# Optimization experiments

Hardware: AMD Instinct MI355X
Metric: run time of the kernel (lower is better)

The kernel has to match this reference:

```python
import jax
import jax.numpy as jnp
import numpy as np

DIM = 1024        # obs dim == latent dim (invertible affine map)
TIME = 4096       # number of timesteps


def setup_inputs() -> dict:
    key = jax.random.key(0)
    ks = jax.random.split(key, 7)
    H = DIM
    scale_hh = 1.0 / np.sqrt(H)
    inp = {
        "ts": jnp.arange(TIME, dtype=jnp.float32),
        "u0": jax.random.normal(ks[0], (H,), dtype=jnp.float32),
        "W_ih": jax.random.normal(ks[1], (3 * H, 1), dtype=jnp.float32) * scale_hh,
        "W_hh": jax.random.normal(ks[2], (3 * H, H), dtype=jnp.float32) * scale_hh,
        "b_ih": jax.random.normal(ks[3], (3 * H,), dtype=jnp.float32) * 0.01,
        "b_hh": jax.random.normal(ks[4], (3 * H,), dtype=jnp.float32) * 0.01,
        # well-conditioned invertible affine map: A = I + 0.02 * N(0,1)
        "A": jnp.eye(H, dtype=jnp.float32)
        + 0.02 * jax.random.normal(ks[5], (H, H), dtype=jnp.float32),
        "c": jax.random.normal(ks[6], (H,), dtype=jnp.float32) * 0.1,
    }
    return inp


def reference(ts, u0, W_ih, W_hh, b_ih, b_hh, A, c):
    # make_initial_state: to_latent(u0) = inverse affine map
    h0 = jnp.linalg.solve(A, u0 - c)  # [H]

    # dim_control is None -> control = zeros(1); input gates are step-invariant
    control = jnp.zeros((1,), dtype=u0.dtype)
    ig = W_ih @ control + b_ih  # [3H]
    ir, iz, inn = jnp.split(ig, 3)

    def gru_cell(h):
        hg = W_hh @ h + b_hh  # [3H]
        hr, hz, hn = jnp.split(hg, 3)
        r = jax.nn.sigmoid(ir + hr)
        z = jax.nn.sigmoid(iz + hz)
        n = jnp.tanh(inn + r * hn)
        return (1.0 - z) * n + z * h

    def body_fn(h_prev, t):
        h_next = gru_cell(h_prev)
        return h_next, h_next

    _, hs_ = jax.lax.scan(body_fn, h0, ts[1:])  # [T-1, H]
    hs = jnp.concatenate((h0[None, :], hs_), axis=0)  # [T, H]

    # vmapped to_obs: affine map obs = A @ h + c
    return hs @ A.T + c  # [T, H]
```

## Files before the change

### kernel.cpp

```cpp
#include <hip/hip_runtime.h>

#define H 1024
#define T 4096
#define GR 64
#define NBLK 256
#define TPB 1024
#define WPB 16
#define SOLVE_ITERS 48
#define FINAL_E (SOLVE_ITERS + T - 1)

typedef float v2f __attribute__((ext_vector_type(2)));
typedef unsigned long long u64;
typedef u64 u64x2 __attribute__((ext_vector_type(2)));

__device__ __forceinline__ float sigmoidf_(float x) { return 1.0f / (1.0f + __expf(-x)); }
__device__ __forceinline__ float tanh_fast_(float x) { return 2.0f * sigmoidf_(2.0f * x) - 1.0f; }

__device__ __forceinline__ u64 pack_(float v, unsigned salt) {
    const unsigned lo = __float_as_uint(v);
    return ((u64)(lo ^ salt) << 32) | lo;
}
__device__ __forceinline__ int valid_(u64 v, unsigned salt) {
    return (((unsigned)(v >> 32)) ^ (unsigned)v) == salt;
}
__device__ __forceinline__ void pub_(u64* p, u64 pk) {
    __hip_atomic_store(p, pk, __ATOMIC_RELAXED, __HIP_MEMORY_SCOPE_AGENT);
}
__device__ __forceinline__ u64x2 load16_coh_(const u64* p) {
    u64x2 v;
    asm volatile("global_load_dwordx4 %0, %1, off sc0 sc1\n\ts_waitcnt vmcnt(0)"
                 : "=v"(v) : "v"(p) : "memory");
    return v;
}
__device__ __forceinline__ u64 load8_coh_(const u64* p) {
    u64 v;
    asm volatile("global_load_dwordx2 %0, %1, off sc0 sc1\n\ts_waitcnt vmcnt(0)"
                 : "=v"(v) : "v"(p) : "memory");
    return v;
}
__device__ __forceinline__ v2f poll2_(const u64* pb, int e, int j2) {
    const unsigned salt = ~(unsigned)e;
    const u64* p = pb + (size_t)(e & 1) * H + j2;
    for (;;) {
        const u64x2 v = load16_coh_(p);
        if (valid_(v.x, salt) && valid_(v.y, salt)) {
            v2f r;
            r.x = __uint_as_float((unsigned)v.x);
            r.y = __uint_as_float((unsigned)v.y);
            return r;
        }
    }
}

__device__ __forceinline__ void rnn_block_(
    const float* __restrict__ u0, const float* __restrict__ W_hh,
    const float* __restrict__ b_ih, const float* __restrict__ b_hh,
    const float* __restrict__ Amat, const float* __restrict__ c,
    float* __restrict__ out, u64* __restrict__ pbuf)
{
    __shared__ float hlds[2][H];
    __shared__ u64 hpub[2][WPB];
    const int tid  = threadIdx.x;
    const int lane = tid & 63;
    const int wave = tid >> 6;
    const int b    = blockIdx.x;
    const int j    = b * WPB + wave;

    float wr[16], wz[16], wn[16];
    {
        const float* pr = W_hh + (size_t)j * H;
        const float* pz = W_hh + (size_t)(H + j) * H;
        const float* pn = W_hh + (size_t)(2 * H + j) * H;
#pragma unroll
        for (int k = 0; k < 16; ++k) {
            wr[k] = pr[lane + 64 * k];
            wz[k] = pz[lane + 64 * k];
            wn[k] = pn[lane + 64 * k];
        }
    }
    const float br  = b_ih[j]         + b_hh[j];
    const float bz  = b_ih[H + j]     + b_hh[H + j];
    const float bin = b_ih[2 * H + j];
    const float bhn = b_hh[2 * H + j];
    const float bj  = u0[j] - c[j];

    if (lane == 0) hpub[0][wave] = pack_(bj, ~0u);
    __syncthreads();
    if (tid < WPB) pub_(&pbuf[(size_t)b * WPB + tid], hpub[0][tid]);

    const float* arow = Amat + (size_t)j * H;
    for (int r = 1; r <= SOLVE_ITERS; ++r) {
        const int pp = (r - 1) & 1;
        if (tid < 512) {
            if ((tid >> 3) == b) {
                const int w0 = 2 * (tid & 7);
                hlds[pp][2 * tid]     = __uint_as_float((unsigned)hpub[pp][w0]);
                hlds[pp][2 * tid + 1] = __uint_as_float((unsigned)hpub[pp][w0 + 1]);
            } else {
                *(v2f*)&hlds[pp][2 * tid] = poll2_(pbuf, r - 1, 2 * tid);
            }
        }
        __syncthreads();
        float acc = 0.f;
#pragma unroll
        for (int k = 0; k < 16; ++k) acc += arow[lane + 64 * k] * hlds[pp][lane + 64 * k];
#pragma unroll
        for (int m = 32; m >= 1; m >>= 1) acc += __shfl_xor(acc, m, 64);
        if (lane == 0) {
            const float hn = bj + hlds[pp][j] - acc;
            hpub[r & 1][wave] = pack_(hn, ~(unsigned)r);
            if (r == SOLVE_ITERS) out[j] = hn;
        }
        __syncthreads();
        if (tid < WPB)
            pub_(&pbuf[(size_t)(r & 1) * H + b * WPB + tid], hpub[r & 1][tid]);
    }

    for (int t = 1; t < T; ++t) {
        const int e  = SOLVE_ITERS + t;
        const int pp = (e - 1) & 1;
        if (tid < 512) {
            if ((tid >> 3) == b) {
                const int w0 = 2 * (tid & 7);
                hlds[pp][2 * tid]     = __uint_as_float((unsigned)hpub[pp][w0]);
                hlds[pp][2 * tid + 1] = __uint_as_float((unsigned)hpub[pp][w0 + 1]);
            } else {
                *(v2f*)&hlds[pp][2 * tid] = poll2_(pbuf, e - 1, 2 * tid);
            }
        }
        __syncthreads();

        float hv[16];
#pragma unroll
        for (int k = 0; k < 16; ++k) hv[k] = hlds[pp][lane + 64 * k];
        float ar = 0.f, az = 0.f, an = 0.f;
#pragma unroll
        for (int k = 0; k < 16; ++k) {
            ar += wr[k] * hv[k];
            az += wz[k] * hv[k];
            an += wn[k] * hv[k];
        }
#pragma unroll
        for (int m = 32; m >= 1; m >>= 1) {
            ar += __shfl_xor(ar, m, 64);
            az += __shfl_xor(az, m, 64);
            an += __shfl_xor(an, m, 64);
        }
        if (lane == 0) {
            const float r2  = sigmoidf_(br + ar);
            const float z2  = sigmoidf_(bz + az);
            const float n2  = tanh_fast_(bin + r2 * (an + bhn));
            const float hn2 = (1.f - z2) * n2 + z2 * hlds[pp][j];
            hpub[e & 1][wave] = pack_(hn2, ~(unsigned)e);
            out[(size_t)t * H + j] = hn2;
        }
        __syncthreads();
        if (tid < WPB)
            pub_(&pbuf[(size_t)(e & 1) * H + b * WPB + tid], hpub[e & 1][tid]);
    }
}

__device__ __forceinline__ void burner_(const u64* __restrict__ pbuf,
                                        float* __restrict__ dummy)
{
    const unsigned salt = ~(unsigned)FINAL_E;
    const u64* flag = &pbuf[(size_t)(FINAL_E & 1) * H];
    const float a = 1.0000001f, b = 1e-7f;
    float x0 = (float)threadIdx.x * 1e-3f + 0.1f;
    float x1 = x0 + 0.25f, x2 = x0 + 0.5f, x3 = x0 + 0.75f;
#pragma unroll 1
    for (int it = 0; it < (1 << 15); ++it) {
#pragma unroll
        for (int k = 0; k < 64; ++k) {
            x0 = __builtin_fmaf(x0, a, b);
            x1 = __builtin_fmaf(x1, a, b);
            x2 = __builtin_fmaf(x2, a, b);
            x3 = __builtin_fmaf(x3, a, b);
        }
        if ((it & 7) == 7) {
            const u64 v = load8_coh_(flag);
            if (valid_(v, salt)) break;
        }
    }
    if (__float_as_uint(x0 + x1 + x2 + x3) == 0xDEADBEEFu)
        dummy[threadIdx.x] = x0;
}

__global__ __launch_bounds__(TPB) void rnn_burn_kernel(
    const float* __restrict__ u0, const float* __restrict__ W_hh,
    const float* __restrict__ b_ih, const float* __restrict__ b_hh,
    const float* __restrict__ A, const float* __restrict__ c,
    float* __restrict__ out, u64* __restrict__ pbuf, float* __restrict__ dummy)
{
    if (blockIdx.x < GR)
        rnn_block_(u0, W_hh, b_ih, b_hh, A, c, out, pbuf);
    else
        burner_(pbuf, dummy);
}

#define ORT 8
__global__ __launch_bounds__(256) void obs_kernel(
    const float* __restrict__ A, const float* __restrict__ c,
    float* __restrict__ out)
{
    __shared__ float hl[ORT][H];
    __shared__ float at[64][65];
    const int tid = threadIdx.x;
    const int t0  = blockIdx.x * ORT;
    for (int i = tid; i < ORT * H / 4; i += 256)
        ((float4*)&hl[0][0])[i] = ((const float4*)(out + (size_t)t0 * H))[i];
    __syncthreads();
    const int li = tid & 63, lt2 = (tid >> 6) * 2;
    for (int it = 0; it < 16; ++it) {
        const int i0 = it * 64;
        float acc0 = c[i0 + li], acc1 = acc0;
        for (int jt = 0; jt < 16; ++jt) {
            const int j0 = jt * 64;
            __syncthreads();
            {
                const int r0 = tid >> 4, cq = (tid & 15) * 4;
                for (int rr = r0; rr < 64; rr += 16) {
                    const float4 v = *(const float4*)&A[(size_t)(i0 + rr) * H + j0 + cq];
                    at[rr][cq] = v.x; at[rr][cq + 1] = v.y;
                    at[rr][cq + 2] = v.z; at[rr][cq + 3] = v.w;
                }
            }
            __syncthreads();
#pragma unroll 16
            for (int jx = 0; jx < 64; ++jx) {
                const float av = at[li][jx];
                acc0 += av * hl[lt2][j0 + jx];
                acc1 += av * hl[lt2 + 1][j0 + jx];
            }
        }
        out[(size_t)(t0 + lt2) * H + i0 + li]     = acc0;
        out[(size_t)(t0 + lt2 + 1) * H + i0 + li] = acc1;
    }
}

extern "C" void kernel_launch(void* const* d_in, const int* in_sizes, int n_in,
                              void* d_out, int out_size, void* d_ws, size_t ws_size,
                              hipStream_t stream) {
    const float* u0   = (const float*)d_in[1];
    const float* W_hh = (const float*)d_in[3];
    const float* b_ih = (const float*)d_in[4];
    const float* b_hh = (const float*)d_in[5];
    const float* A    = (const float*)d_in[6];
    const float* c    = (const float*)d_in[7];
    float* out   = (float*)d_out;
    u64*   pbuf  = (u64*)d_ws;
    float* dummy = (float*)((char*)d_ws + 16384);

    hipLaunchKernelGGL(rnn_burn_kernel, dim3(NBLK), dim3(TPB), 0, stream,
                       u0, W_hh, b_ih, b_hh, A, c, out, pbuf, dummy);
    hipLaunchKernelGGL(obs_kernel, dim3(T / ORT), dim3(256), 0, stream,
                       A, c, out);
}
```

Baseline: 9.915 ms.

## Replace block barriers with salted LDS mailboxes and per-chunk polling

Removes both __syncthreads per timestep. Polling threads write salted 64-bit values into LDS mailboxes, and each wave consumes 64-element chunks as soon as they become valid, accumulating FMAs out of order. Publishing to global memory is done by wave 0 spinning on per-wave salted slots in LDS instead of waiting at a barrier. This aims to cut barrier latency from the serial critical path, but adds LDS spin traffic, bounded timeout loops and a dependence on volatile LDS ordering.

```diff
diff --git a/kernel.cpp b/kernel.cpp
--- a/kernel.cpp
+++ b/kernel.cpp
@@ -38,19 +38,6 @@
                  : "=v"(v) : "v"(p) : "memory");
     return v;
 }
-__device__ __forceinline__ v2f poll2_(const u64* pb, int e, int j2) {
-    const unsigned salt = ~(unsigned)e;
-    const u64* p = pb + (size_t)(e & 1) * H + j2;
-    for (;;) {
-        const u64x2 v = load16_coh_(p);
-        if (valid_(v.x, salt) && valid_(v.y, salt)) {
-            v2f r;
-            r.x = __uint_as_float((unsigned)v.x);
-            r.y = __uint_as_float((unsigned)v.y);
-            return r;
-        }
-    }
-}
 
 __device__ __forceinline__ void rnn_block_(
     const float* __restrict__ u0, const float* __restrict__ W_hh,
@@ -58,13 +45,90 @@
     const float* __restrict__ Amat, const float* __restrict__ c,
     float* __restrict__ out, u64* __restrict__ pbuf)
 {
-    __shared__ float hlds[2][H];
+    __shared__ u64 hmb[2][H];
     __shared__ u64 hpub[2][WPB];
     const int tid  = threadIdx.x;
     const int lane = tid & 63;
     const int wave = tid >> 6;
-    const int b    = blockIdx.x;
-    const int j    = b * WPB + wave;
+    const int bb   = blockIdx.x;
+    const int j    = bb * WPB + wave;
+    const int jl   = j & 63;
+    const int jm   = j >> 6;
+
+    for (int i = tid; i < 2 * H; i += TPB) ((u64*)hmb)[i] = 0ull;
+    if (tid < 2 * WPB) ((u64*)hpub)[tid] = 0ull;
+    __syncthreads();
+
+    const float br  = b_ih[j]         + b_hh[j];
+    const float bz  = b_ih[H + j]     + b_hh[H + j];
+    const float bin = b_ih[2 * H + j];
+    const float bhn = b_hh[2 * H + j];
+    const float bj  = u0[j] - c[j];
+
+    if (lane == 0) hpub[0][wave] = pack_(bj, ~0u);
+    if (wave == 0 && lane < WPB) {
+        const volatile u64* hp = hpub[0];
+        u64 v = hp[lane];
+        int g = 0;
+        while (!valid_(v, ~0u) && ++g < (1 << 22)) v = hp[lane];
+        pub_(&pbuf[(size_t)bb * WPB + lane], v);
+    }
+
+    {
+        float wa[16];
+        const float* arow = Amat + (size_t)j * H;
+#pragma unroll
+        for (int m = 0; m < 16; ++m) wa[m] = arow[lane + 64 * m];
+
+        for (int r = 1; r <= SOLVE_ITERS; ++r) {
+            const int ev = r - 1;
+            const int pc = ev & 1;
+            const unsigned psalt = ~(unsigned)ev;
+            if (tid < 512) {
+                const u64* gp = pbuf + (size_t)pc * H + 2 * tid;
+                u64x2 v; int g = 0;
+                for (;;) {
+                    v = load16_coh_(gp);
+                    if ((valid_(v.x, psalt) && valid_(v.y, psalt)) || ++g > (1 << 20)) break;
+                }
+                hmb[pc][2 * tid]     = v.x;
+                hmb[pc][2 * tid + 1] = v.y;
+            }
+            float acc = 0.f, hself = 0.f;
+            unsigned ok = 0; int g = 0;
+            const volatile u64* hl = hmb[pc];
+            u64 tv[16];
+            while (ok != 0xFFFFu && ++g < (1 << 20)) {
+#pragma unroll
+                for (int m = 0; m < 16; ++m)
+                    if (!(ok >> m & 1)) tv[m] = hl[lane + (m << 6)];
+#pragma unroll
+                for (int m = 0; m < 16; ++m)
+                    if (!(ok >> m & 1) && valid_(tv[m], psalt)) {
+                        ok |= 1u << m;
+                        const float h = __uint_as_float((unsigned)tv[m]);
+                        acc = __builtin_fmaf(wa[m], h, acc);
+                        if (m == jm) hself = h;
+                    }
+            }
+#pragma unroll
+            for (int m = 32; m >= 1; m >>= 1) acc += __shfl_xor(acc, m, 64);
+            const float hpj = __shfl(hself, jl, 64);
+            const float hn  = bj + hpj - acc;
+            if (lane == 0) {
+                hpub[r & 1][wave] = pack_(hn, ~(unsigned)r);
+                if (r == SOLVE_ITERS) out[j] = hn;
+            }
+            if (wave == 0 && lane < WPB) {
+                const volatile u64* hp = hpub[r & 1];
+                const unsigned esalt = ~(unsigned)r;
+                u64 v = hp[lane];
+                int gg = 0;
+                while (!valid_(v, esalt) && ++gg < (1 << 22)) v = hp[lane];
+                pub_(&pbuf[(size_t)(r & 1) * H + bb * WPB + lane], v);
+            }
+        }
+    }
 
     float wr[16], wz[16], wn[16];
     {
@@ -72,73 +136,46 @@
         const float* pz = W_hh + (size_t)(H + j) * H;
         const float* pn = W_hh + (size_t)(2 * H + j) * H;
 #pragma unroll
-        for (int k = 0; k < 16; ++k) {
-            wr[k] = pr[lane + 64 * k];
-            wz[k] = pz[lane + 64 * k];
-            wn[k] = pn[lane + 64 * k];
-        }
-    }
-    const float br  = b_ih[j]         + b_hh[j];
-    const float bz  = b_ih[H + j]     + b_hh[H + j];
-    const float bin = b_ih[2 * H + j];
-    const float bhn = b_hh[2 * H + j];
-    const float bj  = u0[j] - c[j];
-
-    if (lane == 0) hpub[0][wave] = pack_(bj, ~0u);
-    __syncthreads();
-    if (tid < WPB) pub_(&pbuf[(size_t)b * WPB + tid], hpub[0][tid]);
-
-    const float* arow = Amat + (size_t)j * H;
-    for (int r = 1; r <= SOLVE_ITERS; ++r) {
-        const int pp = (r - 1) & 1;
-        if (tid < 512) {
-            if ((tid >> 3) == b) {
-                const int w0 = 2 * (tid & 7);
-                hlds[pp][2 * tid]     = __uint_as_float((unsigned)hpub[pp][w0]);
-                hlds[pp][2 * tid + 1] = __uint_as_float((unsigned)hpub[pp][w0 + 1]);
-            } else {
-                *(v2f*)&hlds[pp][2 * tid] = poll2_(pbuf, r - 1, 2 * tid);
-            }
-        }
-        __syncthreads();
-        float acc = 0.f;
-#pragma unroll
-        for (int k = 0; k < 16; ++k) acc += arow[lane + 64 * k] * hlds[pp][lane + 64 * k];
-#pragma unroll
-        for (int m = 32; m >= 1; m >>= 1) acc += __shfl_xor(acc, m, 64);
-        if (lane == 0) {
-            const float hn = bj + hlds[pp][j] - acc;
-            hpub[r & 1][wave] = pack_(hn, ~(unsigned)r);
-            if (r == SOLVE_ITERS) out[j] = hn;
-        }
-        __syncthreads();
-        if (tid < WPB)
-            pub_(&pbuf[(size_t)(r & 1) * H + b * WPB + tid], hpub[r & 1][tid]);
+        for (int m = 0; m < 16; ++m) {
+            wr[m] = pr[lane + 64 * m];
+            wz[m] = pz[lane + 64 * m];
+            wn[m] = pn[lane + 64 * m];
+        }
     }
 
     for (int t = 1; t < T; ++t) {
         const int e  = SOLVE_ITERS + t;
-        const int pp = (e - 1) & 1;
+        const int ev = e - 1;
+        const int pc = ev & 1;
+        const unsigned psalt = ~(unsigned)ev;
         if (tid < 512) {
-            if ((tid >> 3) == b) {
-                const int w0 = 2 * (tid & 7);
-                hlds[pp][2 * tid]     = __uint_as_float((unsigned)hpub[pp][w0]);
-                hlds[pp][2 * tid + 1] = __uint_as_float((unsigned)hpub[pp][w0 + 1]);
-            } else {
-                *(v2f*)&hlds[pp][2 * tid] = poll2_(pbuf, e - 1, 2 * tid);
-            }
-        }
-        __syncthreads();
-
-        float hv[16];
-#pragma unroll
-        for (int k = 0; k < 16; ++k) hv[k] = hlds[pp][lane + 64 * k];
-        float ar = 0.f, az = 0.f, an = 0.f;
-#pragma unroll
-        for (int k = 0; k < 16; ++k) {
-            ar += wr[k] * hv[k];
-            az += wz[k] * hv[k];
-            an += wn[k] * hv[k];
+            const u64* gp = pbuf + (size_t)pc * H + 2 * tid;
+            u64x2 v; int g = 0;
+            for (;;) {
+                v = load16_coh_(gp);
+                if ((valid_(v.x, psalt) && valid_(v.y, psalt)) || ++g > (1 << 20)) break;
+            }
+            hmb[pc][2 * tid]     = v.x;
+            hmb[pc][2 * tid + 1] = v.y;
+        }
+        float ar = 0.f, az = 0.f, an = 0.f, hself = 0.f;
+        unsigned ok = 0; int g = 0;
+        const volatile u64* hl = hmb[pc];
+        u64 tv[16];
+        while (ok != 0xFFFFu && ++g < (1 << 20)) {
+#pragma unroll
+            for (int m = 0; m < 16; ++m)
+                if (!(ok >> m & 1)) tv[m] = hl[lane + (m << 6)];
+#pragma unroll
+            for (int m = 0; m < 16; ++m)
+                if (!(ok >> m & 1) && valid_(tv[m], psalt)) {
+                    ok |= 1u << m;
+                    const float h = __uint_as_float((unsigned)tv[m]);
+                    ar = __builtin_fmaf(wr[m], h, ar);
+                    az = __builtin_fmaf(wz[m], h, az);
+                    an = __builtin_fmaf(wn[m], h, an);
+                    if (m == jm) hself = h;
+                }
         }
 #pragma unroll
         for (int m = 32; m >= 1; m >>= 1) {
@@ -146,17 +183,23 @@
             az += __shfl_xor(az, m, 64);
             an += __shfl_xor(an, m, 64);
         }
+        const float hpj = __shfl(hself, jl, 64);
+        const float r2  = sigmoidf_(br + ar);
+        const float z2  = sigmoidf_(bz + az);
+        const float n2  = tanh_fast_(bin + r2 * (an + bhn));
+        const float hn2 = (1.f - z2) * n2 + z2 * hpj;
         if (lane == 0) {
-            const float r2  = sigmoidf_(br + ar);
-            const float z2  = sigmoidf_(bz + az);
-            const float n2  = tanh_fast_(bin + r2 * (an + bhn));
-            const float hn2 = (1.f - z2) * n2 + z2 * hlds[pp][j];
             hpub[e & 1][wave] = pack_(hn2, ~(unsigned)e);
             out[(size_t)t * H + j] = hn2;
         }
-        __syncthreads();
-        if (tid < WPB)
-            pub_(&pbuf[(size_t)(e & 1) * H + b * WPB + tid], hpub[e & 1][tid]);
+        if (wave == 0 && lane < WPB) {
+            const volatile u64* hp = hpub[e & 1];
+            const unsigned esalt = ~(unsigned)e;
+            u64 v = hp[lane];
+            int gg = 0;
+            while (!valid_(v, esalt) && ++gg < (1 << 22)) v = hp[lane];
+            pub_(&pbuf[(size_t)(e & 1) * H + bb * WPB + lane], v);
+        }
     }
 }
 
```

New measurement: 25.69 ms. +159.1%, slower.

## Pin recurrent blocks to one XCC and poll with L2-scope loads

Applied to the files above, without the earlier changes.

Doubles the grid and reads the hardware XCC id so that only blocks landing on XCC 0 claim the 64 recurrent slots through an atomic counter; all other blocks run the burner. With every per-step producer and consumer sharing one L2, most polls use L2-coherent loads (sc0) and only every eighth poll is a system-coherent load. The aim is to cut cross-XCC coherence latency on each of the thousands of serial steps. Risks: it assumes exactly 64 co-resident blocks reach XCC 0, the counter is never reset between calls, and the poll loop is now bounded, so it can fall through and return stale values.

```diff
diff --git a/kernel.cpp b/kernel.cpp
--- a/kernel.cpp
+++ b/kernel.cpp
@@ -2,8 +2,7 @@
 
 #define H 1024
 #define T 4096
-#define GR 64
-#define NBLK 256
+#define NBLK 512
 #define TPB 1024
 #define WPB 16
 #define SOLVE_ITERS 48
@@ -32,39 +31,45 @@
                  : "=v"(v) : "v"(p) : "memory");
     return v;
 }
+__device__ __forceinline__ u64x2 load16_l2_(const u64* p) {
+    u64x2 v;
+    asm volatile("global_load_dwordx4 %0, %1, off sc0\n\ts_waitcnt vmcnt(0)"
+                 : "=v"(v) : "v"(p) : "memory");
+    return v;
+}
 __device__ __forceinline__ u64 load8_coh_(const u64* p) {
     u64 v;
     asm volatile("global_load_dwordx2 %0, %1, off sc0 sc1\n\ts_waitcnt vmcnt(0)"
                  : "=v"(v) : "v"(p) : "memory");
     return v;
 }
+
 __device__ __forceinline__ v2f poll2_(const u64* pb, int e, int j2) {
     const unsigned salt = ~(unsigned)e;
     const u64* p = pb + (size_t)(e & 1) * H + j2;
-    for (;;) {
-        const u64x2 v = load16_coh_(p);
-        if (valid_(v.x, salt) && valid_(v.y, salt)) {
-            v2f r;
-            r.x = __uint_as_float((unsigned)v.x);
-            r.y = __uint_as_float((unsigned)v.y);
-            return r;
-        }
-    }
+    u64x2 v;
+    for (int it = 0; it < (1 << 12); ++it) {
+        v = ((it & 7) == 7) ? load16_coh_(p) : load16_l2_(p);
+        if (valid_(v.x, salt) && valid_(v.y, salt)) break;
+    }
+    v2f r;
+    r.x = __uint_as_float((unsigned)v.x);
+    r.y = __uint_as_float((unsigned)v.y);
+    return r;
 }
 
 __device__ __forceinline__ void rnn_block_(
     const float* __restrict__ u0, const float* __restrict__ W_hh,
     const float* __restrict__ b_ih, const float* __restrict__ b_hh,
     const float* __restrict__ Amat, const float* __restrict__ c,
-    float* __restrict__ out, u64* __restrict__ pbuf)
+    float* __restrict__ out, u64* __restrict__ pbuf, const int s)
 {
     __shared__ float hlds[2][H];
     __shared__ u64 hpub[2][WPB];
     const int tid  = threadIdx.x;
     const int lane = tid & 63;
     const int wave = tid >> 6;
-    const int b    = blockIdx.x;
-    const int j    = b * WPB + wave;
+    const int j    = s * WPB + wave;
 
     float wr[16], wz[16], wn[16];
     {
@@ -86,13 +91,13 @@
 
     if (lane == 0) hpub[0][wave] = pack_(bj, ~0u);
     __syncthreads();
-    if (tid < WPB) pub_(&pbuf[(size_t)b * WPB + tid], hpub[0][tid]);
+    if (tid < WPB) pub_(&pbuf[(size_t)s * WPB + tid], hpub[0][tid]);
 
     const float* arow = Amat + (size_t)j * H;
     for (int r = 1; r <= SOLVE_ITERS; ++r) {
         const int pp = (r - 1) & 1;
         if (tid < 512) {
-            if ((tid >> 3) == b) {
+            if ((tid >> 3) == s) {
                 const int w0 = 2 * (tid & 7);
                 hlds[pp][2 * tid]     = __uint_as_float((unsigned)hpub[pp][w0]);
                 hlds[pp][2 * tid + 1] = __uint_as_float((unsigned)hpub[pp][w0 + 1]);
@@ -113,14 +118,14 @@
         }
         __syncthreads();
         if (tid < WPB)
-            pub_(&pbuf[(size_t)(r & 1) * H + b * WPB + tid], hpub[r & 1][tid]);
+            pub_(&pbuf[(size_t)(r & 1) * H + s * WPB + tid], hpub[r & 1][tid]);
     }
 
     for (int t = 1; t < T; ++t) {
         const int e  = SOLVE_ITERS + t;
         const int pp = (e - 1) & 1;
         if (tid < 512) {
-            if ((tid >> 3) == b) {
+            if ((tid >> 3) == s) {
                 const int w0 = 2 * (tid & 7);
                 hlds[pp][2 * tid]     = __uint_as_float((unsigned)hpub[pp][w0]);
                 hlds[pp][2 * tid + 1] = __uint_as_float((unsigned)hpub[pp][w0 + 1]);
@@ -156,7 +161,7 @@
         }
         __syncthreads();
         if (tid < WPB)
-            pub_(&pbuf[(size_t)(e & 1) * H + b * WPB + tid], hpub[e & 1][tid]);
+            pub_(&pbuf[(size_t)(e & 1) * H + s * WPB + tid], hpub[e & 1][tid]);
     }
 }
 
@@ -186,14 +191,25 @@
         dummy[threadIdx.x] = x0;
 }
 
-__global__ __launch_bounds__(TPB) void rnn_burn_kernel(
+__global__ __launch_bounds__(TPB, 8) void rnn_burn_kernel(
     const float* __restrict__ u0, const float* __restrict__ W_hh,
     const float* __restrict__ b_ih, const float* __restrict__ b_hh,
     const float* __restrict__ A, const float* __restrict__ c,
-    float* __restrict__ out, u64* __restrict__ pbuf, float* __restrict__ dummy)
-{
-    if (blockIdx.x < GR)
-        rnn_block_(u0, W_hh, b_ih, b_hh, A, c, out, pbuf);
+    float* __restrict__ out, u64* __restrict__ pbuf, float* __restrict__ dummy,
+    unsigned* __restrict__ ctl)
+{
+    __shared__ int slot_s;
+    if (threadIdx.x == 0) {
+        unsigned xcc;
+        asm volatile("s_getreg_b32 %0, hwreg(HW_REG_XCC_ID)" : "=s"(xcc));
+        int s = -1;
+        if (xcc == 0) s = (int)(atomicAdd(ctl, 1u) & 63u);
+        slot_s = s;
+    }
+    __syncthreads();
+    const int s = slot_s;
+    if (s >= 0)
+        rnn_block_(u0, W_hh, b_ih, b_hh, A, c, out, pbuf, s);
     else
         burner_(pbuf, dummy);
 }
@@ -250,9 +266,10 @@
     float* out   = (float*)d_out;
     u64*   pbuf  = (u64*)d_ws;
     float* dummy = (float*)((char*)d_ws + 16384);
+    unsigned* ctl = (unsigned*)((char*)d_ws + 20480);
 
     hipLaunchKernelGGL(rnn_burn_kernel, dim3(NBLK), dim3(TPB), 0, stream,
-                       u0, W_hh, b_ih, b_hh, A, c, out, pbuf, dummy);
+                       u0, W_hh, b_ih, b_hh, A, c, out, pbuf, dummy, ctl);
     hipLaunchKernelGGL(obs_kernel, dim3(T / ORT), dim3(256), 0, stream,
                        A, c, out);
 }
```

New measurement: 27.42 ms. +176.6%, slower.
